# Kernel tuning notes

Measured on AMD Instinct MI355X. Metric: run time of the kernel, lower is better.

Reference implementation:

```python
import jax, jax.numpy as jnp
import numpy as np

N = 1536       # n_nodes
D_IN = 256     # in_features
D_OUT = 64     # out_features (= n_hidden, n_heads=1, is_concat=True)
N_WAY = 16     # known_attacks_count
SLOPE = 0.2    # LeakyReLU negative slope


def setup_inputs() -> dict:
    key = jax.random.key(0)
    k1, k2, k3, k4, k5 = jax.random.split(key, 5)
    hidden_vectors = jax.random.normal(k1, (N, D_IN), dtype=jnp.float32)
    labels = jax.random.randint(k2, (N, 1), 0, N_WAY)
    zda_mask = jax.random.randint(k3, (N, 1), 0, 2).astype(bool)
    # deterministic support/query split: first half support, last half query
    query_mask = jnp.concatenate([jnp.zeros(N // 2, bool), jnp.ones(N // 2, bool)])
    W = jax.random.normal(k4, (D_OUT, D_IN), jnp.float32) * (1.0 / np.sqrt(D_IN))
    attn_w = jax.random.normal(k5, (D_OUT,), jnp.float32) * (1.0 / np.sqrt(D_OUT))
    return {"hidden_vectors": hidden_vectors, "W": W, "attn_w": attn_w,
            "labels": labels, "zda_mask": zda_mask, "query_mask": query_mask,
            "known_attacks_count": N_WAY}


def _forward(hidden_vectors, W, attn_w, labels, zda_mask, n_way):
    n = hidden_vectors.shape[0]
    dt = hidden_vectors.dtype
    # one-hot labels (scatter equivalent)
    oh = jax.nn.one_hot(labels[:, 0], n_way, dtype=dt)                 # [n, n_way]
    known = ~zda_mask[:, 0]                                            # unknown == zda
    ohm = jnp.where(known[:, None], oh, jnp.zeros((), dt))             # masked one-hot
    # collaborative kernel: semantic similarity between known pairs, else 1
    sem = ohm @ ohm.T                                                  # [n, n]
    cond = known[:, None] & known[None, :]
    kernel = jnp.where(cond, sem, jnp.ones((), dt))
    # GATv2 with shared weights, 1 head: e[i,j] = attn . lrelu(g[i] + g[j])
    g = hidden_vectors @ W.T                                           # [n, d_out]
    s = g[:, None, :] + g[None, :, :]                                  # [n, n, d_out]
    s = jnp.where(s >= 0, s, SLOPE * s)                                # LeakyReLU
    e = jnp.einsum('ijd,d->ij', s, attn_w)                             # [n, n]
    e = jnp.where(kernel == 0.0, -jnp.inf, e)                          # colaborative mask
    a = jax.nn.softmax(e, axis=1)                                      # [n, n]
    h_out = a @ g                                                      # [n, d_out] (concat, 1 head)
    # centroids over support nodes (first half)
    n_sup = n // 2
    h_sup, oh_sup = h_out[:n_sup], oh[:n_sup]
    agg = oh_sup.T @ h_sup                                             # [n_way, d_out]
    counts = oh_sup.sum(0)                                             # [n_way]
    centroids = jnp.where((counts > 0)[:, None],
                          agg / jnp.maximum(counts, 1.0)[:, None], 0.0)
    # inverse euclidean distance scores for query nodes (last half)
    hq = h_out[n_sup:]
    d2 = (jnp.sum(hq * hq, 1)[:, None] + jnp.sum(centroids * centroids, 1)[None, :]
          - 2.0 * hq @ centroids.T)
    dist = jnp.sqrt(jnp.maximum(d2, 0.0))
    scores = 1.0 / (dist + 1e-10)
    return scores, h_out, a


def reference(hidden_vectors, W, attn_w, labels, zda_mask, query_mask, known_attacks_count):
    return _forward(hidden_vectors, W, attn_w, labels, zda_mask, known_attacks_count)
```

## Files before the change

kernel.cpp:

```cpp
#include <hip/hip_runtime.h>
#include <math.h>

#define NN 1536
#define DIN 256
#define DOUT 64
#define NWAY 16
#define NSUP 768
#define IB 12
#define JBLK 128
#define SROWS 6

#define OFF_SCORES 0
#define OFF_H 12288
#define OFF_A 110592

#define WG 0
#define WQ 98304
#define WCODE 99840
#define WCENT 101376

__global__ __launch_bounds__(256) void k_g(const float* __restrict__ hid,
                                           const float* __restrict__ W,
                                           const float* __restrict__ attw,
                                           const int* __restrict__ labels,
                                           const int* __restrict__ zda,
                                           float* __restrict__ g,
                                           float* __restrict__ q,
                                           int* __restrict__ code) {
  int t = threadIdx.x;
  int r = t >> 6, d = t & 63;
  int i = blockIdx.x * 4 + r;
  const float4* hp = (const float4*)(hid + (size_t)i * DIN);
  const float4* wp = (const float4*)(W + (size_t)d * DIN);
  float4 acc = {0.f, 0.f, 0.f, 0.f};
#pragma unroll
  for (int k = 0; k < DIN / 4; k++) {
    float4 h4 = hp[k];
    float4 w4 = wp[k];
    acc.x = fmaf(h4.x, w4.x, acc.x);
    acc.y = fmaf(h4.y, w4.y, acc.y);
    acc.z = fmaf(h4.z, w4.z, acc.z);
    acc.w = fmaf(h4.w, w4.w, acc.w);
  }
  float gv = (acc.x + acc.y) + (acc.z + acc.w);
  g[(size_t)i * DOUT + d] = gv;
  float val = gv * attw[d];
#pragma unroll
  for (int off = 32; off >= 1; off >>= 1) val += __shfl_xor(val, off, 64);
  if (d == 0) q[i] = 0.6f * val;
  if (t < 4) {
    int ii = blockIdx.x * 4 + t;
    code[ii] = zda[ii] ? -1 : labels[ii];
  }
}

__global__ __launch_bounds__(256, 3) void k_e(const float* __restrict__ g,
                                              const float* __restrict__ q,
                                              const int* __restrict__ code,
                                              const float* __restrict__ attw,
                                              float* __restrict__ aout) {
  __shared__ float gis[IB * DOUT];
  __shared__ float lds_p[4][IB][64];
  __shared__ float qi[IB];
  __shared__ int ci[IB];
  int t = threadIdx.x;
  int lane = t & 63;
  int w = t >> 6;
  int whalf = __builtin_amdgcn_readfirstlane(w & 1);
  int jhi = w >> 1;
  int i0 = blockIdx.x * IB;
  int j0 = blockIdx.y * JBLK;
  int j = j0 + jhi * 64 + lane;

  if (t < IB * 16) {
    ((float4*)gis)[t] = ((const float4*)(g + (size_t)i0 * DOUT))[t];
  } else if (t < IB * 16 + IB) {
    int u = t - IB * 16;
    qi[u] = q[i0 + u];
    ci[u] = code[i0 + u];
  }
  float4 gj[8];
  const float4* gp = (const float4*)(g + (size_t)j * DOUT + whalf * 32);
#pragma unroll
  for (int k = 0; k < 8; k++) gj[k] = gp[k];
  const float4* wv = (const float4*)(attw + whalf * 32);
  __syncthreads();

#pragma unroll 1
  for (int u = 0; u < IB; u++) {
    const float4* gv = (const float4*)(gis + u * DOUT + whalf * 32);
    float4 acc = {0.f, 0.f, 0.f, 0.f};
#pragma unroll
    for (int k = 0; k < 8; k++) {
      float4 a4 = gv[k];
      float4 w4 = wv[k];
      float4 b4 = gj[k];
      acc.x = fmaf(w4.x, fabsf(a4.x + b4.x), acc.x);
      acc.y = fmaf(w4.y, fabsf(a4.y + b4.y), acc.y);
      acc.z = fmaf(w4.z, fabsf(a4.z + b4.z), acc.z);
      acc.w = fmaf(w4.w, fabsf(a4.w + b4.w), acc.w);
    }
    lds_p[w][u][lane] = (acc.x + acc.y) + (acc.z + acc.w);
  }
  __syncthreads();

  int jl = t & 127;
  int sb = (jl >> 6) * 2;
  int ll = jl & 63;
  int jg = j0 + jl;
  float qj = q[jg];
  int cj = code[jg];
  int u0 = (t >> 7) * 6;
#pragma unroll
  for (int v = 0; v < 6; v++) {
    int u = u0 + v;
    float s = lds_p[sb][u][ll] + lds_p[sb + 1][u][ll];
    float e = (qi[u] + qj) + 0.4f * s;
    int cu = ci[u];
    if ((cu >= 0) && (cj >= 0) && (cu != cj)) e = -1e30f;
    aout[(size_t)(i0 + u) * NN + jg] = e;
  }
}

__global__ __launch_bounds__(512) void k_smh(float* __restrict__ a,
                                             const float* __restrict__ g,
                                             float* __restrict__ h) {
  __shared__ float al[SROWS][NN];
  __shared__ float part[32][SROWS][68];
  __shared__ float red[16];
  int t = threadIdx.x;
  int lane = t & 63;
  int w = t >> 6;
  int r0 = blockIdx.x * SROWS;

#pragma unroll 1
  for (int r = 0; r < SROWS; r++) {
    float* row = a + (size_t)(r0 + r) * NN;
    float v0 = row[t], v1 = row[t + 512], v2 = row[t + 1024];
    float m = fmaxf(fmaxf(v0, v1), v2);
#pragma unroll
    for (int off = 32; off >= 1; off >>= 1) m = fmaxf(m, __shfl_xor(m, off, 64));
    if (lane == 0) red[w] = m;
    __syncthreads();
    m = red[0];
#pragma unroll
    for (int k = 1; k < 8; k++) m = fmaxf(m, red[k]);
    v0 = __expf(v0 - m);
    v1 = __expf(v1 - m);
    v2 = __expf(v2 - m);
    float s = (v0 + v1) + v2;
#pragma unroll
    for (int off = 32; off >= 1; off >>= 1) s += __shfl_xor(s, off, 64);
    if (lane == 0) red[8 + w] = s;
    __syncthreads();
    s = red[8];
#pragma unroll
    for (int k = 1; k < 8; k++) s += red[8 + k];
    float inv = 1.f / s;
    v0 *= inv; v1 *= inv; v2 *= inv;
    al[r][t] = v0; al[r][t + 512] = v1; al[r][t + 1024] = v2;
    row[t] = v0; row[t + 512] = v1; row[t + 1024] = v2;
    __syncthreads();
  }

  int jr = t >> 4;
  int dq = t & 15;
  float4 acc0 = {0,0,0,0}, acc1 = {0,0,0,0}, acc2 = {0,0,0,0};
  float4 acc3 = {0,0,0,0}, acc4 = {0,0,0,0}, acc5 = {0,0,0,0};
#pragma unroll 4
  for (int jj = 0; jj < NN / 32; jj++) {
    int j = jj * 32 + jr;
    float4 g4 = *(const float4*)(g + (size_t)j * DOUT + dq * 4);
    float a0 = al[0][j], a1 = al[1][j], a2 = al[2][j];
    float a3 = al[3][j], a4 = al[4][j], a5 = al[5][j];
    acc0.x = fmaf(a0, g4.x, acc0.x); acc0.y = fmaf(a0, g4.y, acc0.y);
    acc0.z = fmaf(a0, g4.z, acc0.z); acc0.w = fmaf(a0, g4.w, acc0.w);
    acc1.x = fmaf(a1, g4.x, acc1.x); acc1.y = fmaf(a1, g4.y, acc1.y);
    acc1.z = fmaf(a1, g4.z, acc1.z); acc1.w = fmaf(a1, g4.w, acc1.w);
    acc2.x = fmaf(a2, g4.x, acc2.x); acc2.y = fmaf(a2, g4.y, acc2.y);
    acc2.z = fmaf(a2, g4.z, acc2.z); acc2.w = fmaf(a2, g4.w, acc2.w);
    acc3.x = fmaf(a3, g4.x, acc3.x); acc3.y = fmaf(a3, g4.y, acc3.y);
    acc3.z = fmaf(a3, g4.z, acc3.z); acc3.w = fmaf(a3, g4.w, acc3.w);
    acc4.x = fmaf(a4, g4.x, acc4.x); acc4.y = fmaf(a4, g4.y, acc4.y);
    acc4.z = fmaf(a4, g4.z, acc4.z); acc4.w = fmaf(a4, g4.w, acc4.w);
    acc5.x = fmaf(a5, g4.x, acc5.x); acc5.y = fmaf(a5, g4.y, acc5.y);
    acc5.z = fmaf(a5, g4.z, acc5.z); acc5.w = fmaf(a5, g4.w, acc5.w);
  }
  *(float4*)(&part[jr][0][dq * 4]) = acc0;
  *(float4*)(&part[jr][1][dq * 4]) = acc1;
  *(float4*)(&part[jr][2][dq * 4]) = acc2;
  *(float4*)(&part[jr][3][dq * 4]) = acc3;
  *(float4*)(&part[jr][4][dq * 4]) = acc4;
  *(float4*)(&part[jr][5][dq * 4]) = acc5;
  __syncthreads();
  if (t < SROWS * DOUT) {
    int r = t >> 6, d = t & 63;
    float s = 0.f;
#pragma unroll
    for (int k = 0; k < 32; k++) s += part[k][r][d];
    h[(size_t)(r0 + r) * DOUT + d] = s;
  }
}

__global__ __launch_bounds__(1024) void k_cent(const float* __restrict__ h,
                                               const int* __restrict__ labels,
                                               float* __restrict__ cent) {
  __shared__ float part[16][64];
  __shared__ int pc[16];
  int c = blockIdx.x, t = threadIdx.x;
  int d = t & 63, rq = t >> 6;
  float acc = 0.f;
  int cnt = 0;
#pragma unroll 4
  for (int r = rq; r < NSUP; r += 16) {
    int lab = labels[r];
    if (lab == c) { acc += h[(size_t)r * DOUT + d]; cnt++; }
  }
  part[rq][d] = acc;
  if (d == 0) pc[rq] = cnt;
  __syncthreads();
  if (t < 64) {
    float num = 0.f;
    int count = 0;
#pragma unroll
    for (int k = 0; k < 16; k++) { num += part[k][t]; count += pc[k]; }
    cent[c * DOUT + t] = (count > 0) ? (num / (float)count) : 0.f;
  }
}

__global__ __launch_bounds__(256) void k_scores(const float* __restrict__ h,
                                                const float* __restrict__ cent,
                                                float* __restrict__ scores) {
  __shared__ float cl[NWAY * 65];
  __shared__ float hl[16 * 65];
  int t = threadIdx.x;
  int q0 = blockIdx.x * 16;
#pragma unroll
  for (int u = 0; u < 4; u++) {
    int f = t + u * 256;
    int row = f >> 6, k = f & 63;
    cl[row * 65 + k] = cent[f];
    hl[row * 65 + k] = h[(size_t)(NSUP + q0) * DOUT + f];
  }
  __syncthreads();
  int qr = t >> 4, c = t & 15;
  const float* hv = hl + qr * 65;
  const float* cv = cl + c * 65;
  float hh = 0.f, cc = 0.f, hc = 0.f;
#pragma unroll
  for (int k = 0; k < DOUT; k++) {
    float av = hv[k], bv = cv[k];
    hh = fmaf(av, av, hh);
    cc = fmaf(bv, bv, cc);
    hc = fmaf(av, bv, hc);
  }
  float d2 = fmaxf(hh + cc - 2.f * hc, 0.f);
  scores[q0 * NWAY + t] = 1.f / (sqrtf(d2) + 1e-10f);
}

extern "C" void kernel_launch(void* const* d_in, const int* in_sizes, int n_in,
                              void* d_out, int out_size, void* d_ws, size_t ws_size,
                              hipStream_t stream) {
  const float* hid = (const float*)d_in[0];
  const float* W = (const float*)d_in[1];
  const float* attw = (const float*)d_in[2];
  const int* labels = (const int*)d_in[3];
  const int* zda = (const int*)d_in[4];
  float* out = (float*)d_out;
  float* ws = (float*)d_ws;

  float* g = ws + WG;
  float* q = ws + WQ;
  int* code = (int*)(ws + WCODE);
  float* cent = ws + WCENT;
  float* scores = out + OFF_SCORES;
  float* h = out + OFF_H;
  float* a = out + OFF_A;

  hipLaunchKernelGGL(k_g, dim3(NN / 4), dim3(256), 0, stream, hid, W, attw, labels, zda, g, q, code);
  hipLaunchKernelGGL(k_e, dim3(NN / IB, NN / JBLK), dim3(256), 0, stream, g, q, code, attw, a);
  hipLaunchKernelGGL(k_smh, dim3(NN / SROWS), dim3(512), 0, stream, a, g, h);
  hipLaunchKernelGGL(k_cent, dim3(NWAY), dim3(1024), 0, stream, h, labels, cent);
  hipLaunchKernelGGL(k_scores, dim3(NSUP / 16), dim3(256), 0, stream, h, cent, scores);
}
```

Before: 72.01 us.

## Fuse attention logits, softmax and aggregation into one kernel

Merges the logit kernel and the softmax+aggregation kernel into a single 1024-thread kernel. Each block computes six full rows of logits into LDS, applies the softmax in place, and writes the attention matrix to global once. It then aggregates h with wave shuffles instead of an LDS partial reduction. This removes the write-then-reread of the 9 MB logit matrix and one launch, at the cost of only 256 large blocks with heavy LDS use and less parallelism in the logit phase.

New measurement: 82.04 us. +13.9%, slower.

```diff
diff --git a/kernel.cpp b/kernel.cpp
--- a/kernel.cpp
+++ b/kernel.cpp
@@ -6,9 +6,7 @@
 #define DOUT 64
 #define NWAY 16
 #define NSUP 768
-#define IB 12
-#define JBLK 128
-#define SROWS 6
+#define MR 6
 
 #define OFF_SCORES 0
 #define OFF_H 12288
@@ -54,125 +52,124 @@
   }
 }
 
-__global__ __launch_bounds__(256, 3) void k_e(const float* __restrict__ g,
+__global__ __launch_bounds__(1024) void k_esh(const float* __restrict__ g,
                                               const float* __restrict__ q,
                                               const int* __restrict__ code,
                                               const float* __restrict__ attw,
-                                              float* __restrict__ aout) {
-  __shared__ float gis[IB * DOUT];
-  __shared__ float lds_p[4][IB][64];
-  __shared__ float qi[IB];
-  __shared__ int ci[IB];
+                                              float* __restrict__ aout,
+                                              float* __restrict__ hout) {
+  __shared__ float el[MR][NN];
+  __shared__ float lp[16][MR][64];
+  __shared__ float gis[MR * DOUT];
+  __shared__ float qi[MR];
+  __shared__ int ci[MR];
+  __shared__ float redm[16];
+  __shared__ float reds[16];
+
   int t = threadIdx.x;
   int lane = t & 63;
   int w = t >> 6;
-  int whalf = __builtin_amdgcn_readfirstlane(w & 1);
-  int jhi = w >> 1;
-  int i0 = blockIdx.x * IB;
-  int j0 = blockIdx.y * JBLK;
-  int j = j0 + jhi * 64 + lane;
-
-  if (t < IB * 16) {
+  int i0 = blockIdx.x * MR;
+
+  if (t < MR * 16) {
     ((float4*)gis)[t] = ((const float4*)(g + (size_t)i0 * DOUT))[t];
-  } else if (t < IB * 16 + IB) {
-    int u = t - IB * 16;
+  } else if (t < MR * 16 + MR) {
+    int u = t - MR * 16;
     qi[u] = q[i0 + u];
     ci[u] = code[i0 + u];
   }
-  float4 gj[8];
-  const float4* gp = (const float4*)(g + (size_t)j * DOUT + whalf * 32);
-#pragma unroll
-  for (int k = 0; k < 8; k++) gj[k] = gp[k];
+  int whalf = __builtin_amdgcn_readfirstlane(w & 1);
+  int jgrp = w >> 1;
   const float4* wv = (const float4*)(attw + whalf * 32);
   __syncthreads();
 
 #pragma unroll 1
-  for (int u = 0; u < IB; u++) {
-    const float4* gv = (const float4*)(gis + u * DOUT + whalf * 32);
-    float4 acc = {0.f, 0.f, 0.f, 0.f};
-#pragma unroll
-    for (int k = 0; k < 8; k++) {
-      float4 a4 = gv[k];
-      float4 w4 = wv[k];
-      float4 b4 = gj[k];
-      acc.x = fmaf(w4.x, fabsf(a4.x + b4.x), acc.x);
-      acc.y = fmaf(w4.y, fabsf(a4.y + b4.y), acc.y);
-      acc.z = fmaf(w4.z, fabsf(a4.z + b4.z), acc.z);
-      acc.w = fmaf(w4.w, fabsf(a4.w + b4.w), acc.w);
+  for (int p = 0; p < 3; p++) {
+    int j = p * 512 + jgrp * 64 + lane;
+    float4 gj[8];
+    const float4* gp = (const float4*)(g + (size_t)j * DOUT + whalf * 32);
+#pragma unroll
+    for (int k = 0; k < 8; k++) gj[k] = gp[k];
+#pragma unroll 1
+    for (int u = 0; u < MR; u++) {
+      const float4* gv = (const float4*)(gis + u * DOUT + whalf * 32);
+      float4 acc = {0.f, 0.f, 0.f, 0.f};
+#pragma unroll
+      for (int k = 0; k < 8; k++) {
+        float4 a4 = gv[k];
+        float4 w4 = wv[k];
+        float4 b4 = gj[k];
+        acc.x = fmaf(w4.x, fabsf(a4.x + b4.x), acc.x);
+        acc.y = fmaf(w4.y, fabsf(a4.y + b4.y), acc.y);
+        acc.z = fmaf(w4.z, fabsf(a4.z + b4.z), acc.z);
+        acc.w = fmaf(w4.w, fabsf(a4.w + b4.w), acc.w);
+      }
+      lp[w][u][lane] = (acc.x + acc.y) + (acc.z + acc.w);
     }
-    lds_p[w][u][lane] = (acc.x + acc.y) + (acc.z + acc.w);
-  }
-  __syncthreads();
-
-  int jl = t & 127;
-  int sb = (jl >> 6) * 2;
-  int ll = jl & 63;
-  int jg = j0 + jl;
-  float qj = q[jg];
-  int cj = code[jg];
-  int u0 = (t >> 7) * 6;
-#pragma unroll
-  for (int v = 0; v < 6; v++) {
-    int u = u0 + v;
-    float s = lds_p[sb][u][ll] + lds_p[sb + 1][u][ll];
-    float e = (qi[u] + qj) + 0.4f * s;
-    int cu = ci[u];
-    if ((cu >= 0) && (cj >= 0) && (cu != cj)) e = -1e30f;
-    aout[(size_t)(i0 + u) * NN + jg] = e;
-  }
-}
-
-__global__ __launch_bounds__(512) void k_smh(float* __restrict__ a,
-                                             const float* __restrict__ g,
-                                             float* __restrict__ h) {
-  __shared__ float al[SROWS][NN];
-  __shared__ float part[32][SROWS][68];
-  __shared__ float red[16];
-  int t = threadIdx.x;
-  int lane = t & 63;
-  int w = t >> 6;
-  int r0 = blockIdx.x * SROWS;
+    __syncthreads();
+    {
+      int jsl = t & 511;
+      int jgc = jsl >> 6;
+      int ln = jsl & 63;
+      int jglob = p * 512 + jsl;
+      float qj = q[jglob];
+      int cj = code[jglob];
+      int u0 = (t >> 9) * 3;
+#pragma unroll
+      for (int v = 0; v < 3; v++) {
+        int u = u0 + v;
+        float s = lp[jgc * 2][u][ln] + lp[jgc * 2 + 1][u][ln];
+        float e = (qi[u] + qj) + 0.4f * s;
+        int cu = ci[u];
+        if ((cu >= 0) && (cj >= 0) && (cu != cj)) e = -1e30f;
+        el[u][jglob] = e;
+      }
+    }
+    __syncthreads();
+  }
 
 #pragma unroll 1
-  for (int r = 0; r < SROWS; r++) {
-    float* row = a + (size_t)(r0 + r) * NN;
-    float v0 = row[t], v1 = row[t + 512], v2 = row[t + 1024];
-    float m = fmaxf(fmaxf(v0, v1), v2);
+  for (int r = 0; r < MR; r++) {
+    float v0 = el[r][t];
+    float v1 = (t < 512) ? el[r][1024 + t] : -3.0e38f;
+    float m = fmaxf(v0, v1);
 #pragma unroll
     for (int off = 32; off >= 1; off >>= 1) m = fmaxf(m, __shfl_xor(m, off, 64));
-    if (lane == 0) red[w] = m;
-    __syncthreads();
-    m = red[0];
-#pragma unroll
-    for (int k = 1; k < 8; k++) m = fmaxf(m, red[k]);
-    v0 = __expf(v0 - m);
-    v1 = __expf(v1 - m);
-    v2 = __expf(v2 - m);
-    float s = (v0 + v1) + v2;
+    if (lane == 0) redm[w] = m;
+    __syncthreads();
+    m = redm[0];
+#pragma unroll
+    for (int k = 1; k < 16; k++) m = fmaxf(m, redm[k]);
+    float e0 = __expf(v0 - m);
+    float e1 = (t < 512) ? __expf(v1 - m) : 0.f;
+    float s = e0 + e1;
 #pragma unroll
     for (int off = 32; off >= 1; off >>= 1) s += __shfl_xor(s, off, 64);
-    if (lane == 0) red[8 + w] = s;
-    __syncthreads();
-    s = red[8];
-#pragma unroll
-    for (int k = 1; k < 8; k++) s += red[8 + k];
+    if (lane == 0) reds[w] = s;
+    __syncthreads();
+    s = reds[0];
+#pragma unroll
+    for (int k = 1; k < 16; k++) s += reds[k];
     float inv = 1.f / s;
-    v0 *= inv; v1 *= inv; v2 *= inv;
-    al[r][t] = v0; al[r][t + 512] = v1; al[r][t + 1024] = v2;
-    row[t] = v0; row[t + 512] = v1; row[t + 1024] = v2;
-    __syncthreads();
-  }
-
-  int jr = t >> 4;
-  int dq = t & 15;
+    e0 *= inv;
+    el[r][t] = e0;
+    aout[(size_t)(i0 + r) * NN + t] = e0;
+    if (t < 512) {
+      e1 *= inv;
+      el[r][1024 + t] = e1;
+      aout[(size_t)(i0 + r) * NN + 1024 + t] = e1;
+    }
+  }
+  __syncthreads();
+
   float4 acc0 = {0,0,0,0}, acc1 = {0,0,0,0}, acc2 = {0,0,0,0};
   float4 acc3 = {0,0,0,0}, acc4 = {0,0,0,0}, acc5 = {0,0,0,0};
 #pragma unroll 4
-  for (int jj = 0; jj < NN / 32; jj++) {
-    int j = jj * 32 + jr;
-    float4 g4 = *(const float4*)(g + (size_t)j * DOUT + dq * 4);
-    float a0 = al[0][j], a1 = al[1][j], a2 = al[2][j];
-    float a3 = al[3][j], a4 = al[4][j], a5 = al[5][j];
+  for (int jj = 0; jj < NN / 64; jj++) {
+    int j = jj * 64 + lane;
+    float4 g4 = *(const float4*)(g + (size_t)j * DOUT + w * 4);
+    float a0 = el[0][j], a1 = el[1][j], a2 = el[2][j];
+    float a3 = el[3][j], a4 = el[4][j], a5 = el[5][j];
     acc0.x = fmaf(a0, g4.x, acc0.x); acc0.y = fmaf(a0, g4.y, acc0.y);
     acc0.z = fmaf(a0, g4.z, acc0.z); acc0.w = fmaf(a0, g4.w, acc0.w);
     acc1.x = fmaf(a1, g4.x, acc1.x); acc1.y = fmaf(a1, g4.y, acc1.y);
@@ -186,19 +183,28 @@
     acc5.x = fmaf(a5, g4.x, acc5.x); acc5.y = fmaf(a5, g4.y, acc5.y);
     acc5.z = fmaf(a5, g4.z, acc5.z); acc5.w = fmaf(a5, g4.w, acc5.w);
   }
-  *(float4*)(&part[jr][0][dq * 4]) = acc0;
-  *(float4*)(&part[jr][1][dq * 4]) = acc1;
-  *(float4*)(&part[jr][2][dq * 4]) = acc2;
-  *(float4*)(&part[jr][3][dq * 4]) = acc3;
-  *(float4*)(&part[jr][4][dq * 4]) = acc4;
-  *(float4*)(&part[jr][5][dq * 4]) = acc5;
-  __syncthreads();
-  if (t < SROWS * DOUT) {
-    int r = t >> 6, d = t & 63;
-    float s = 0.f;
-#pragma unroll
-    for (int k = 0; k < 32; k++) s += part[k][r][d];
-    h[(size_t)(r0 + r) * DOUT + d] = s;
+#pragma unroll
+  for (int off = 32; off >= 1; off >>= 1) {
+    acc0.x += __shfl_xor(acc0.x, off, 64); acc0.y += __shfl_xor(acc0.y, off, 64);
+    acc0.z += __shfl_xor(acc0.z, off, 64); acc0.w += __shfl_xor(acc0.w, off, 64);
+    acc1.x += __shfl_xor(acc1.x, off, 64); acc1.y += __shfl_xor(acc1.y, off, 64);
+    acc1.z += __shfl_xor(acc1.z, off, 64); acc1.w += __shfl_xor(acc1.w, off, 64);
+    acc2.x += __shfl_xor(acc2.x, off, 64); acc2.y += __shfl_xor(acc2.y, off, 64);
+    acc2.z += __shfl_xor(acc2.z, off, 64); acc2.w += __shfl_xor(acc2.w, off, 64);
+    acc3.x += __shfl_xor(acc3.x, off, 64); acc3.y += __shfl_xor(acc3.y, off, 64);
+    acc3.z += __shfl_xor(acc3.z, off, 64); acc3.w += __shfl_xor(acc3.w, off, 64);
+    acc4.x += __shfl_xor(acc4.x, off, 64); acc4.y += __shfl_xor(acc4.y, off, 64);
+    acc4.z += __shfl_xor(acc4.z, off, 64); acc4.w += __shfl_xor(acc4.w, off, 64);
+    acc5.x += __shfl_xor(acc5.x, off, 64); acc5.y += __shfl_xor(acc5.y, off, 64);
+    acc5.z += __shfl_xor(acc5.z, off, 64); acc5.w += __shfl_xor(acc5.w, off, 64);
+  }
+  if (lane == 0) {
+    *(float4*)(hout + (size_t)(i0 + 0) * DOUT + w * 4) = acc0;
+    *(float4*)(hout + (size_t)(i0 + 1) * DOUT + w * 4) = acc1;
+    *(float4*)(hout + (size_t)(i0 + 2) * DOUT + w * 4) = acc2;
+    *(float4*)(hout + (size_t)(i0 + 3) * DOUT + w * 4) = acc3;
+    *(float4*)(hout + (size_t)(i0 + 4) * DOUT + w * 4) = acc4;
+    *(float4*)(hout + (size_t)(i0 + 5) * DOUT + w * 4) = acc5;
   }
 }
 
@@ -278,8 +284,7 @@
   float* a = out + OFF_A;
 
   hipLaunchKernelGGL(k_g, dim3(NN / 4), dim3(256), 0, stream, hid, W, attw, labels, zda, g, q, code);
-  hipLaunchKernelGGL(k_e, dim3(NN / IB, NN / JBLK), dim3(256), 0, stream, g, q, code, attw, a);
-  hipLaunchKernelGGL(k_smh, dim3(NN / SROWS), dim3(512), 0, stream, a, g, h);
+  hipLaunchKernelGGL(k_esh, dim3(NN / MR), dim3(1024), 0, stream, g, q, code, attw, a, h);
   hipLaunchKernelGGL(k_cent, dim3(NWAY), dim3(1024), 0, stream, h, labels, cent);
   hipLaunchKernelGGL(k_scores, dim3(NSUP / 16), dim3(256), 0, stream, h, cent, scores);
 }
```
